# Kernel optimization log

Hardware: AMD Instinct MI355X
Metric: run time of the kernel (lower is better)

Reference implementation:

```python
import jax, jax.numpy as jnp
import numpy as np

R, B, S, H, E, P = 8, 16, 512, 1024, 32, 4  # roles, batch, seq(=max_seq_len=char_len), hidden, entities, spans/entity


def setup_inputs() -> dict:
    key = jax.random.key(0)
    ks = jax.random.split(key, 12)
    w = 0.02
    return {
        "role_labels": jax.random.randint(ks[0], (R, B), 0, S),
        "summar_role_embedding": jax.random.normal(ks[1], (R, B, S, H), jnp.float32),
        "token_embedding": jax.random.normal(ks[2], (B, S, H), jnp.float32),
        "entities_embedding": jax.random.normal(ks[3], (B, S, H), jnp.float32),
        "token_mask": jnp.ones((B, S), jnp.float32),
        "entity_mask": jnp.ones((B, S), jnp.float32),
        # padded ragged spans: sort (start,end) so start<=end; empty spans write nothing
        "entity_spans": jnp.sort(jax.random.randint(ks[4], (B, E, P, 2), 0, S), axis=-1),
        # -1 encodes Python None entries in the original ragged maps
        "char2token": jax.random.randint(ks[5], (B, S), -1, S),
        "entity2token": jax.random.randint(ks[6], (B, S), -1, E),
        "single_w": jax.random.normal(ks[7], (3 * H, 1), jnp.float32) * w,
        "single_b": jnp.zeros((1,), jnp.float32),
        "multi_w": jax.random.normal(ks[8], (3 * H, 1), jnp.float32) * w,
        "multi_b": jnp.zeros((1,), jnp.float32),
        "answer_w": jax.random.normal(ks[9], (2 * H, H), jnp.float32) * w,
        "answer_b": jnp.zeros((H,), jnp.float32),
    }


def reference(role_labels, summar_role_embedding, token_embedding, entities_embedding,
              token_mask, entity_mask, entity_spans, char2token, entity2token,
              single_w, single_b, multi_w, multi_b, answer_w, answer_b):
    Bd, Sd, Hd = token_embedding.shape
    Ed = entity_spans.shape[1]
    brow = jnp.arange(Bd)[:, None]
    cvalid = char2token >= 0
    cidx = jnp.where(cvalid, char2token, 0)
    evalid = entity2token >= 0
    eidx = jnp.where(evalid, entity2token, 0)
    pos = jnp.arange(Sd)[None, None, None, :]  # [1,1,1,S]
    # span coverage mask [B,E,P,S]; assumes non-overlapping gold spans (matches sequential writes)
    cover = ((pos >= entity_spans[..., 0:1]) & (pos < entity_spans[..., 1:2])).astype(token_embedding.dtype)
    mask_sum = token_mask.sum()

    def step(pre_answer, xs):
        sr_emb, labels = xs
        s_logit = jnp.concatenate([sr_emb, token_embedding, pre_answer], -1) @ single_w + single_b  # [B,S,1]
        m_logit = jnp.concatenate([sr_emb, entities_embedding, pre_answer], -1) @ multi_w + multi_b
        # nn.Softmax() with no dim on a 3D tensor uses legacy dim=0 (batch axis)
        s_pred = jax.nn.softmax(s_logit, axis=0)[..., 0]  # [B,S]
        m_pred = jax.nn.softmax(m_logit, axis=0)[..., 0]
        # scatter-add char scores onto token positions / entity ids
        pred_token_ids = jnp.zeros((Bd, Sd), s_pred.dtype).at[brow, cidx].add(jnp.where(cvalid, s_pred, 0.0))
        entity_scores = jnp.zeros((Bd, Ed), m_pred.dtype).at[brow, eidx].add(jnp.where(evalid, m_pred, 0.0))
        # broadcast entity score over its spans
        pred_entity_ids = jnp.einsum('beps,be->bs', cover, entity_scores)
        merged = jnp.maximum(pred_token_ids, pred_entity_ids)  # max-merge [B,S]
        # gather merged scores back to char positions
        arg_emb = jnp.where(cvalid, jnp.take_along_axis(merged, cidx, axis=1), 0.0)[..., None]  # [B,S,1]
        curr = token_embedding * arg_emb
        new_pre = jnp.concatenate([curr, pre_answer], -1) @ answer_w + answer_b
        # CrossEntropyLoss(merged [B,C=S], labels [B]) -> scalar mean, then * token_mask.sum()
        nll = -jnp.take_along_axis(jax.nn.log_softmax(merged, -1), labels[:, None], axis=1).mean()
        return new_pre, (merged, nll * mask_sum)

    pre0 = jnp.zeros_like(token_embedding)
    _, (pred_arg_ids, losses) = jax.lax.scan(step, pre0, (summar_role_embedding, role_labels))
    return losses.sum(), pred_arg_ids
```

## Files before the change

kernel.cpp:

```cpp
#include <hip/hip_runtime.h>
#include <stdint.h>

#define R_ 8
#define B_ 16
#define S_ 512
#define H_ 1024
#define E_ 32
#define P_ 4
#define M_ (B_*S_)
#define NWAVE_ 4096

__device__ __forceinline__ float dot4(float4 a, float4 b){
  return a.x*b.x + a.y*b.y + a.z*b.z + a.w*b.w;
}

__global__ __launch_bounds__(256) void vec_chain_kernel(
    int k, const float* __restrict__ aw, const float* __restrict__ ab,
    const float* __restrict__ sw, const float* __restrict__ mw,
    float* __restrict__ a_s, float* __restrict__ a_m,
    float* __restrict__ V, float* __restrict__ betas)
{
  int w = (int)((blockIdx.x * blockDim.x + threadIdx.x) >> 6);
  int lane = threadIdx.x & 63;
  const float* as_k = (k == 0) ? (sw + 2*H_) : (a_s + (size_t)k*H_);
  const float* am_k = (k == 0) ? (mw + 2*H_) : (a_m + (size_t)k*H_);
  if (w < H_){
    const float* w1 = aw + (size_t)w * H_;
    const float* w2 = aw + (size_t)(H_ + w) * H_;
    float vs = 0.f, vm = 0.f, ns = 0.f, nm = 0.f;
    #pragma unroll
    for (int i = 0; i < 4; i++){
      int c = i*256 + lane*4;
      float4 r1 = *(const float4*)(w1 + c);
      float4 r2 = *(const float4*)(w2 + c);
      float4 xs = *(const float4*)(as_k + c);
      float4 xm = *(const float4*)(am_k + c);
      vs += dot4(r1, xs); vm += dot4(r1, xm);
      ns += dot4(r2, xs); nm += dot4(r2, xm);
    }
    #pragma unroll
    for (int m = 32; m >= 1; m >>= 1){
      vs += __shfl_xor(vs, m, 64); vm += __shfl_xor(vm, m, 64);
      ns += __shfl_xor(ns, m, 64); nm += __shfl_xor(nm, m, 64);
    }
    if (lane == 0){
      V[(size_t)k*H_ + w]       = vs;
      V[(size_t)(7 + k)*H_ + w] = vm;
      a_s[(size_t)(k+1)*H_ + w] = ns;
      a_m[(size_t)(k+1)*H_ + w] = nm;
    }
  } else if (w == H_ || w == H_ + 1){
    const float* av = (w == H_) ? as_k : am_k;
    float d = 0.f;
    #pragma unroll
    for (int i = 0; i < 4; i++){
      int c = i*256 + lane*4;
      d += dot4(*(const float4*)(ab + c), *(const float4*)(av + c));
    }
    #pragma unroll
    for (int m = 32; m >= 1; m >>= 1) d += __shfl_xor(d, m, 64);
    if (lane == 0) betas[(w == H_ ? 0 : 8) + k] = d;
  }
}

__global__ __launch_bounds__(256, 4) void dots_all_kernel(
    const float* __restrict__ sr, const float* __restrict__ tok,
    const float* __restrict__ ent, const float* __restrict__ sw,
    const float* __restrict__ mw, const float* __restrict__ V,
    const float* __restrict__ tmask,
    float* __restrict__ sr_s, float* __restrict__ sr_m,
    float* __restrict__ tok_s, float* __restrict__ ent_m,
    float* __restrict__ G, float* __restrict__ PS,
    float* __restrict__ msum, float* __restrict__ out)
{
  const int gtid = blockIdx.x * 256 + threadIdx.x;
  const int gw   = gtid >> 6;
  const int lane = threadIdx.x & 63;
  const int co   = lane * 4;

  if (gtid < 32768) ((float4*)PS)[gtid] = make_float4(0.f,0.f,0.f,0.f);
  if (gw == 0){
    float s = 0.f;
    #pragma unroll
    for (int i = 0; i < 32; i++){
      float4 v = ((const float4*)tmask)[i*64 + lane];
      s += v.x + v.y + v.z + v.w;
    }
    #pragma unroll
    for (int m = 32; m >= 1; m >>= 1) s += __shfl_xor(s, m, 64);
    if (lane == 0){ msum[0] = s; out[0] = 0.f; }
  }

  {
    float4 ws[4], wm[4];
    #pragma unroll
    for (int i = 0; i < 4; i++){
      ws[i] = *(const float4*)(sw + i*256 + co);
      wm[i] = *(const float4*)(mw + i*256 + co);
    }
    float4 bufA[8], bufB[8];
    auto LDP = [&](float4* buf, int p){
      const float* r0 = sr + (size_t)p * (2*H_);
      #pragma unroll
      for (int i = 0; i < 4; i++){
        buf[i]   = *(const float4*)(r0 + i*256 + co);
        buf[4+i] = *(const float4*)(r0 + H_ + i*256 + co);
      }
    };
    auto CMP = [&](const float4* buf, int p){
      float a0=0.f,a1=0.f,b0=0.f,b1=0.f;
      #pragma unroll
      for (int i = 0; i < 4; i++){
        a0 += dot4(buf[i],   ws[i]);  a1 += dot4(buf[i],   wm[i]);
        b0 += dot4(buf[4+i], ws[i]);  b1 += dot4(buf[4+i], wm[i]);
      }
      #pragma unroll
      for (int m = 32; m >= 1; m >>= 1){
        a0 += __shfl_xor(a0,m,64); a1 += __shfl_xor(a1,m,64);
        b0 += __shfl_xor(b0,m,64); b1 += __shfl_xor(b1,m,64);
      }
      if (lane == 0){
        sr_s[2*p]   = a0; sr_m[2*p]   = a1;
        sr_s[2*p+1] = b0; sr_m[2*p+1] = b1;
      }
    };
    LDP(bufA, gw);
    #pragma unroll
    for (int it = 0; it < 8; it += 2){
      LDP(bufB, gw + (it+1)*NWAVE_);
      CMP(bufA, gw + it*NWAVE_);
      if (it + 2 < 8) LDP(bufA, gw + (it+2)*NWAVE_);
      CMP(bufB, gw + (it+1)*NWAVE_);
    }
  }

  {
    const int h  = gw & 1;
    const int r0 = gw >> 1;
    float4 vA[4], vB[4];
    auto LDV = [&](float4* v, int rr){
      const float* rp = tok + (size_t)rr * H_;
      #pragma unroll
      for (int i = 0; i < 4; i++) v[i] = *(const float4*)(rp + i*256 + co);
    };
    if (h == 0){
      auto CMP0 = [&](const float4* v, int rr){
        float acc[8] = {};
        #pragma unroll
        for (int i = 0; i < 4; i++){
          int c = i*256 + co;
          acc[0] += dot4(v[i], *(const float4*)(sw + H_ + c));
          #pragma unroll
          for (int q = 0; q < 7; q++)
            acc[q+1] += dot4(v[i], *(const float4*)(V + (size_t)q*H_ + c));
        }
        #pragma unroll
        for (int m = 32; m >= 1; m >>= 1)
          #pragma unroll
          for (int q = 0; q < 8; q++) acc[q] += __shfl_xor(acc[q],m,64);
        if (lane == 0){
          tok_s[rr] = acc[0];
          #pragma unroll
          for (int q = 0; q < 7; q++) G[(size_t)q*M_ + rr] = acc[q+1];
        }
      };
      LDV(vA, r0);
      LDV(vB, r0 + 2048); CMP0(vA, r0);
      LDV(vA, r0 + 4096); CMP0(vB, r0 + 2048);
      LDV(vB, r0 + 6144); CMP0(vA, r0 + 4096);
      CMP0(vB, r0 + 6144);
    } else {
      auto CMP1 = [&](const float4* v, int rr){
        float acc[7] = {};
        #pragma unroll
        for (int i = 0; i < 4; i++){
          int c = i*256 + co;
          #pragma unroll
          for (int q = 0; q < 7; q++)
            acc[q] += dot4(v[i], *(const float4*)(V + (size_t)(7+q)*H_ + c));
        }
        #pragma unroll
        for (int m = 32; m >= 1; m >>= 1)
          #pragma unroll
          for (int q = 0; q < 7; q++) acc[q] += __shfl_xor(acc[q],m,64);
        if (lane == 0){
          #pragma unroll
          for (int q = 0; q < 7; q++) G[(size_t)(7+q)*M_ + rr] = acc[q];
        }
      };
      LDV(vA, r0);
      LDV(vB, r0 + 2048); CMP1(vA, r0);
      LDV(vA, r0 + 4096); CMP1(vB, r0 + 2048);
      LDV(vB, r0 + 6144); CMP1(vA, r0 + 4096);
      CMP1(vB, r0 + 6144);
    }
  }

  {
    float4 wmh[4];
    #pragma unroll
    for (int i = 0; i < 4; i++) wmh[i] = *(const float4*)(mw + H_ + i*256 + co);
    float4 eA[4], eB[4];
    const float* rpA = ent + (size_t)gw * H_;
    const float* rpB = ent + (size_t)(gw + 4096) * H_;
    #pragma unroll
    for (int i = 0; i < 4; i++) eA[i] = *(const float4*)(rpA + i*256 + co);
    #pragma unroll
    for (int i = 0; i < 4; i++) eB[i] = *(const float4*)(rpB + i*256 + co);
    float a0 = 0.f, b0 = 0.f;
    #pragma unroll
    for (int i = 0; i < 4; i++){ a0 += dot4(eA[i], wmh[i]); b0 += dot4(eB[i], wmh[i]); }
    #pragma unroll
    for (int m = 32; m >= 1; m >>= 1){ a0 += __shfl_xor(a0,m,64); b0 += __shfl_xor(b0,m,64); }
    if (lane == 0){ ent_m[gw] = a0; ent_m[gw + 4096] = b0; }
  }
}

__global__ __launch_bounds__(512) void role_kernel(
    int r,
    const float* __restrict__ sr_s, const float* __restrict__ sr_m,
    const float* __restrict__ tok_s, const float* __restrict__ ent_m,
    const float* __restrict__ G, const float* __restrict__ betas,
    const float* __restrict__ sb, const float* __restrict__ mb,
    const int* __restrict__ c2t, const int* __restrict__ e2t,
    const int* __restrict__ spans, const int* __restrict__ labels,
    const float* __restrict__ msum, float* __restrict__ out,
    float* __restrict__ xlog, float* __restrict__ PS)
{
  __shared__ float pta[S_];
  __shared__ float merged[S_];
  __shared__ float es[E_];
  __shared__ float red[8];
  __shared__ int   spn[E_*P_*2];
  const int b = blockIdx.x;
  const int t = threadIdx.x;
  const int bs = b*S_ + t;
  const int wid = t >> 6, lane = t & 63;

  pta[t] = 0.f;
  if (t < E_) es[t] = 0.f;
  if (t < E_*P_*2) spn[t] = spans[b*(E_*P_*2) + t];
  const int c_own = c2t[bs];
  const int e_own = e2t[bs];

  float sl[B_], ml[B_];
  if (r == 0){
    const float sb0 = sb[0], mb0 = mb[0];
    #pragma unroll
    for (int bb = 0; bb < B_; bb++){
      int q = bb*S_ + t;
      sl[bb] = sr_s[q] + tok_s[q] + sb0;
      ml[bb] = sr_m[q] + ent_m[q] + mb0;
    }
  } else {
    const float* xc = xlog + (size_t)(r & 1) * (2*M_);
    #pragma unroll
    for (int bb = 0; bb < B_; bb++){
      sl[bb] = xc[bb*S_ + t];
      ml[bb] = xc[M_ + bb*S_ + t];
    }
  }
  float smax = -1e30f, mmax = -1e30f;
  #pragma unroll
  for (int bb = 0; bb < B_; bb++){ smax = fmaxf(smax, sl[bb]); mmax = fmaxf(mmax, ml[bb]); }
  float ssum = 0.f, msv = 0.f;
  #pragma unroll
  for (int bb = 0; bb < B_; bb++){ ssum += __expf(sl[bb]-smax); msv += __expf(ml[bb]-mmax); }
  float spv = __expf(sl[b]-smax) / ssum;
  float mpv = __expf(ml[b]-mmax) / msv;

  __syncthreads();
  if (c_own >= 0) atomicAdd(&pta[c_own], spv);
  if (e_own >= 0) atomicAdd(&es[e_own], mpv);
  __syncthreads();

  float pei = 0.f;
  #pragma unroll
  for (int e = 0; e < E_; e++){
    float sc = es[e];
    #pragma unroll
    for (int p = 0; p < P_; p++){
      int st = spn[e*8 + p*2], en = spn[e*8 + p*2 + 1];
      if (t >= st && t < en) pei += sc;
    }
  }
  float mg = fmaxf(pta[t], pei);
  merged[t] = mg;
  out[1 + (size_t)r*M_ + bs] = mg;
  __syncthreads();

  float ah_r = (c_own >= 0) ? merged[c_own] : 0.f;

  float mx = mg;
  #pragma unroll
  for (int k = 32; k >= 1; k >>= 1) mx = fmaxf(mx, __shfl_xor(mx, k, 64));
  if (lane == 0) red[wid] = mx;
  __syncthreads();
  float gmx = red[0];
  #pragma unroll
  for (int i = 1; i < 8; i++) gmx = fmaxf(gmx, red[i]);
  float se = __expf(mg - gmx);
  #pragma unroll
  for (int k = 32; k >= 1; k >>= 1) se += __shfl_xor(se, k, 64);
  __syncthreads();
  if (lane == 0) red[wid] = se;
  __syncthreads();
  if (t == 0){
    float tot = 0.f;
    #pragma unroll
    for (int i = 0; i < 8; i++) tot += red[i];
    float lse = gmx + __logf(tot);
    int lbl = labels[r*B_ + b];
    float nll = lse - merged[lbl];
    atomicAdd(out, nll * msum[0] * (1.0f/16.0f));
  }

  if (r < 7){
    float ps_next = 0.f, pm_next = 0.f;
    for (int q = r + 1; q <= 7; q++){
      float gs = G[(size_t)(q-1-r)*M_ + bs];
      float gm = G[(size_t)(7 + q-1-r)*M_ + bs];
      float ns = PS[((size_t)q*2 + 0)*M_ + bs] + ah_r * gs;
      float nm = PS[((size_t)q*2 + 1)*M_ + bs] + ah_r * gm;
      PS[((size_t)q*2 + 0)*M_ + bs] = ns;
      PS[((size_t)q*2 + 1)*M_ + bs] = nm;
      if (q == r + 1){ ps_next = ns; pm_next = nm; }
    }
    float bsum_s = 0.f, bsum_m = 0.f;
    for (int k = 0; k <= r; k++){ bsum_s += betas[k]; bsum_m += betas[8 + k]; }
    float xn = sr_s[(size_t)((r+1)*B_ + b)*S_ + t] + tok_s[bs] + ps_next + sb[0] + bsum_s;
    float yn = sr_m[(size_t)((r+1)*B_ + b)*S_ + t] + ent_m[bs] + pm_next + mb[0] + bsum_m;
    float* xn_buf = xlog + (size_t)((r+1) & 1) * (2*M_);
    xn_buf[bs] = xn;
    xn_buf[M_ + bs] = yn;
  }
}

extern "C" void kernel_launch(void* const* d_in, const int* in_sizes, int n_in,
                              void* d_out, int out_size, void* d_ws, size_t ws_size,
                              hipStream_t stream){
  (void)in_sizes; (void)n_in; (void)out_size; (void)ws_size;
  const int*   labels = (const int*)  d_in[0];
  const float* sr     = (const float*)d_in[1];
  const float* tok    = (const float*)d_in[2];
  const float* ent    = (const float*)d_in[3];
  const float* tmask  = (const float*)d_in[4];
  const int*   spans  = (const int*)  d_in[6];
  const int*   c2t    = (const int*)  d_in[7];
  const int*   e2t    = (const int*)  d_in[8];
  const float* sw     = (const float*)d_in[9];
  const float* sb     = (const float*)d_in[10];
  const float* mw     = (const float*)d_in[11];
  const float* mb     = (const float*)d_in[12];
  const float* aw     = (const float*)d_in[13];
  const float* ab     = (const float*)d_in[14];
  float* out = (float*)d_out;
  char*  ws  = (char*)d_ws;

  size_t o = 0;
  auto take = [&](size_t bytes){ size_t c = o; o += (bytes + 255) & ~(size_t)255; return c; };
  float* sr_s  = (float*)(ws + take((size_t)R_*B_*S_*4));
  float* sr_m  = (float*)(ws + take((size_t)R_*B_*S_*4));
  float* tok_s = (float*)(ws + take((size_t)B_*S_*4));
  float* ent_m = (float*)(ws + take((size_t)B_*S_*4));
  float* a_s   = (float*)(ws + take((size_t)8*H_*4));
  float* a_m   = (float*)(ws + take((size_t)8*H_*4));
  float* V     = (float*)(ws + take((size_t)14*H_*4));
  float* betas = (float*)(ws + take(64));
  float* G     = (float*)(ws + take((size_t)14*M_*4));
  float* PS    = (float*)(ws + take((size_t)8*2*M_*4));
  float* xlog  = (float*)(ws + take((size_t)2*2*M_*4));
  float* msum  = (float*)(ws + take(256));

  for (int k = 0; k < 7; k++)
    vec_chain_kernel<<<257, 256, 0, stream>>>(k, aw, ab, sw, mw, a_s, a_m, V, betas);
  dots_all_kernel<<<1024, 256, 0, stream>>>(sr, tok, ent, sw, mw, V, tmask,
                                            sr_s, sr_m, tok_s, ent_m, G, PS, msum, out);
  for (int r = 0; r < R_; r++){
    role_kernel<<<16, 512, 0, stream>>>(r, sr_s, sr_m, tok_s, ent_m, G, betas,
                                        sb, mb, c2t, e2t, spans, labels, msum, out,
                                        xlog, PS);
  }
}
```

Measured before the change: 187.0 us.

## Fuse vector chain into streaming kernel with grid barriers; persistent role loop

Folds the seven sequential vec_chain launches into a mega kernel: 64 blocks run the matrix-vector chain with software grid barriers, then compute the token dot products against V. The remaining blocks stream the role and entity embeddings at the same time. The eight role launches become one persistent 16-block kernel that loops over roles with an inter-block barrier. This removes about fifteen launch gaps and overlaps the dependent chain with bandwidth-bound work. The cost is spin-wait barriers that assume all blocks are co-resident, and fewer waves left for the token dot products.

New measurement: 487.5 us. 2.61x slower.

```diff
diff --git a/kernel.cpp b/kernel.cpp
--- a/kernel.cpp
+++ b/kernel.cpp
@@ -8,95 +8,140 @@
 #define E_ 32
 #define P_ 4
 #define M_ (B_*S_)
-#define NWAVE_ 4096
+#define CHAINB_ 64
+#define TOTB_ 1024
+#define SRW_ ((TOTB_-CHAINB_)*4)
 
 __device__ __forceinline__ float dot4(float4 a, float4 b){
   return a.x*b.x + a.y*b.y + a.z*b.z + a.w*b.w;
 }
 
-__global__ __launch_bounds__(256) void vec_chain_kernel(
-    int k, const float* __restrict__ aw, const float* __restrict__ ab,
-    const float* __restrict__ sw, const float* __restrict__ mw,
-    float* __restrict__ a_s, float* __restrict__ a_m,
-    float* __restrict__ V, float* __restrict__ betas)
-{
-  int w = (int)((blockIdx.x * blockDim.x + threadIdx.x) >> 6);
-  int lane = threadIdx.x & 63;
-  const float* as_k = (k == 0) ? (sw + 2*H_) : (a_s + (size_t)k*H_);
-  const float* am_k = (k == 0) ? (mw + 2*H_) : (a_m + (size_t)k*H_);
-  if (w < H_){
-    const float* w1 = aw + (size_t)w * H_;
-    const float* w2 = aw + (size_t)(H_ + w) * H_;
-    float vs = 0.f, vm = 0.f, ns = 0.f, nm = 0.f;
-    #pragma unroll
-    for (int i = 0; i < 4; i++){
-      int c = i*256 + lane*4;
-      float4 r1 = *(const float4*)(w1 + c);
-      float4 r2 = *(const float4*)(w2 + c);
-      float4 xs = *(const float4*)(as_k + c);
-      float4 xm = *(const float4*)(am_k + c);
-      vs += dot4(r1, xs); vm += dot4(r1, xm);
-      ns += dot4(r2, xs); nm += dot4(r2, xm);
-    }
-    #pragma unroll
-    for (int m = 32; m >= 1; m >>= 1){
-      vs += __shfl_xor(vs, m, 64); vm += __shfl_xor(vm, m, 64);
-      ns += __shfl_xor(ns, m, 64); nm += __shfl_xor(nm, m, 64);
-    }
-    if (lane == 0){
-      V[(size_t)k*H_ + w]       = vs;
-      V[(size_t)(7 + k)*H_ + w] = vm;
-      a_s[(size_t)(k+1)*H_ + w] = ns;
-      a_m[(size_t)(k+1)*H_ + w] = nm;
-    }
-  } else if (w == H_ || w == H_ + 1){
-    const float* av = (w == H_) ? as_k : am_k;
-    float d = 0.f;
-    #pragma unroll
-    for (int i = 0; i < 4; i++){
-      int c = i*256 + lane*4;
-      d += dot4(*(const float4*)(ab + c), *(const float4*)(av + c));
-    }
-    #pragma unroll
-    for (int m = 32; m >= 1; m >>= 1) d += __shfl_xor(d, m, 64);
-    if (lane == 0) betas[(w == H_ ? 0 : 8) + k] = d;
+__device__ __forceinline__ void group_barrier(int* cnt, int nblk){
+  __syncthreads();
+  if (threadIdx.x == 0){
+    __threadfence();
+    __hip_atomic_fetch_add(cnt, 1, __ATOMIC_RELEASE, __HIP_MEMORY_SCOPE_AGENT);
+    while (__hip_atomic_load(cnt, __ATOMIC_ACQUIRE, __HIP_MEMORY_SCOPE_AGENT) < nblk)
+      __builtin_amdgcn_s_sleep(8);
+    __threadfence();
   }
-}
-
-__global__ __launch_bounds__(256, 4) void dots_all_kernel(
+  __syncthreads();
+}
+
+__global__ __launch_bounds__(256, 4) void mega_kernel(
     const float* __restrict__ sr, const float* __restrict__ tok,
     const float* __restrict__ ent, const float* __restrict__ sw,
-    const float* __restrict__ mw, const float* __restrict__ V,
-    const float* __restrict__ tmask,
+    const float* __restrict__ mw, const float* __restrict__ aw,
+    const float* __restrict__ ab, const float* __restrict__ tmask,
     float* __restrict__ sr_s, float* __restrict__ sr_m,
     float* __restrict__ tok_s, float* __restrict__ ent_m,
+    float* __restrict__ a_s, float* __restrict__ a_m,
+    float* __restrict__ V, float* __restrict__ betas,
     float* __restrict__ G, float* __restrict__ PS,
-    float* __restrict__ msum, float* __restrict__ out)
+    float* __restrict__ msum, float* __restrict__ out, int* bar)
 {
-  const int gtid = blockIdx.x * 256 + threadIdx.x;
-  const int gw   = gtid >> 6;
+  const int blk  = blockIdx.x;
   const int lane = threadIdx.x & 63;
+  const int lw   = threadIdx.x >> 6;
   const int co   = lane * 4;
 
-  if (gtid < 32768) ((float4*)PS)[gtid] = make_float4(0.f,0.f,0.f,0.f);
-  if (gw == 0){
-    float s = 0.f;
-    #pragma unroll
-    for (int i = 0; i < 32; i++){
-      float4 v = ((const float4*)tmask)[i*64 + lane];
-      s += v.x + v.y + v.z + v.w;
-    }
-    #pragma unroll
-    for (int m = 32; m >= 1; m >>= 1) s += __shfl_xor(s, m, 64);
-    if (lane == 0){ msum[0] = s; out[0] = 0.f; }
-  }
-
-  {
-    float4 ws[4], wm[4];
+  if (blk < CHAINB_){
+    const int cw = blk*4 + lw;
+    for (int k = 0; k < 7; ++k){
+      const float* as_k = (k==0) ? (sw + 2*H_) : (a_s + (size_t)k*H_);
+      const float* am_k = (k==0) ? (mw + 2*H_) : (a_m + (size_t)k*H_);
+      float4 xs[4], xm[4];
+      #pragma unroll
+      for (int i = 0; i < 4; i++){
+        xs[i] = *(const float4*)(as_k + i*256 + co);
+        xm[i] = *(const float4*)(am_k + i*256 + co);
+      }
+      #pragma unroll
+      for (int rr = 0; rr < 4; ++rr){
+        int w = cw*4 + rr;
+        const float* w1 = aw + (size_t)w * H_;
+        const float* w2 = aw + (size_t)(H_ + w) * H_;
+        float vs=0.f, vm=0.f, ns=0.f, nm=0.f;
+        #pragma unroll
+        for (int i = 0; i < 4; i++){
+          float4 r1 = *(const float4*)(w1 + i*256 + co);
+          float4 r2 = *(const float4*)(w2 + i*256 + co);
+          vs += dot4(r1, xs[i]); vm += dot4(r1, xm[i]);
+          ns += dot4(r2, xs[i]); nm += dot4(r2, xm[i]);
+        }
+        #pragma unroll
+        for (int m = 32; m >= 1; m >>= 1){
+          vs += __shfl_xor(vs,m,64); vm += __shfl_xor(vm,m,64);
+          ns += __shfl_xor(ns,m,64); nm += __shfl_xor(nm,m,64);
+        }
+        if (lane == 0){
+          V[(size_t)k*H_ + w]       = vs;
+          V[(size_t)(7+k)*H_ + w]   = vm;
+          a_s[(size_t)(k+1)*H_ + w] = ns;
+          a_m[(size_t)(k+1)*H_ + w] = nm;
+        }
+      }
+      if (cw == 0){
+        float d0=0.f, d1=0.f;
+        #pragma unroll
+        for (int i = 0; i < 4; i++){
+          float4 r = *(const float4*)(ab + i*256 + co);
+          d0 += dot4(r, xs[i]); d1 += dot4(r, xm[i]);
+        }
+        #pragma unroll
+        for (int m = 32; m >= 1; m >>= 1){ d0+=__shfl_xor(d0,m,64); d1+=__shfl_xor(d1,m,64); }
+        if (lane == 0){ betas[k] = d0; betas[8+k] = d1; }
+      }
+      group_barrier(&bar[k], CHAINB_);
+    }
+    for (int it = 0; it < 32; ++it){
+      int rr = cw + it*256;
+      const float* rp = tok + (size_t)rr * H_;
+      float4 v[4];
+      #pragma unroll
+      for (int i = 0; i < 4; i++) v[i] = *(const float4*)(rp + i*256 + co);
+      float acc[15];
+      #pragma unroll
+      for (int q = 0; q < 15; q++) acc[q] = 0.f;
+      #pragma unroll
+      for (int i = 0; i < 4; i++){
+        int c = i*256 + co;
+        acc[0] += dot4(v[i], *(const float4*)(sw + H_ + c));
+        #pragma unroll
+        for (int q = 0; q < 14; q++)
+          acc[q+1] += dot4(v[i], *(const float4*)(V + (size_t)q*H_ + c));
+      }
+      #pragma unroll
+      for (int m = 32; m >= 1; m >>= 1)
+        #pragma unroll
+        for (int q = 0; q < 15; q++) acc[q] += __shfl_xor(acc[q],m,64);
+      if (lane == 0){
+        tok_s[rr] = acc[0];
+        #pragma unroll
+        for (int q = 0; q < 14; q++) G[(size_t)q*M_ + rr] = acc[q+1];
+      }
+    }
+  } else {
+    const int sb   = blk - CHAINB_;
+    const int swv  = sb*4 + lw;
+    const int gtid2 = sb*256 + threadIdx.x;
+    if (gtid2 < 32768) ((float4*)PS)[gtid2] = make_float4(0.f,0.f,0.f,0.f);
+    if (swv == 0){
+      float s = 0.f;
+      #pragma unroll
+      for (int i = 0; i < 32; i++){
+        float4 vv = ((const float4*)tmask)[i*64 + lane];
+        s += vv.x + vv.y + vv.z + vv.w;
+      }
+      #pragma unroll
+      for (int m = 32; m >= 1; m >>= 1) s += __shfl_xor(s,m,64);
+      if (lane == 0){ msum[0] = s; out[0] = 0.f; }
+    }
+    float4 ws4[4], wm4[4];
     #pragma unroll
     for (int i = 0; i < 4; i++){
-      ws[i] = *(const float4*)(sw + i*256 + co);
-      wm[i] = *(const float4*)(mw + i*256 + co);
+      ws4[i] = *(const float4*)(sw + i*256 + co);
+      wm4[i] = *(const float4*)(mw + i*256 + co);
     }
     float4 bufA[8], bufB[8];
     auto LDP = [&](float4* buf, int p){
@@ -111,113 +156,51 @@
       float a0=0.f,a1=0.f,b0=0.f,b1=0.f;
       #pragma unroll
       for (int i = 0; i < 4; i++){
-        a0 += dot4(buf[i],   ws[i]);  a1 += dot4(buf[i],   wm[i]);
-        b0 += dot4(buf[4+i], ws[i]);  b1 += dot4(buf[4+i], wm[i]);
+        a0 += dot4(buf[i],   ws4[i]);  a1 += dot4(buf[i],   wm4[i]);
+        b0 += dot4(buf[4+i], ws4[i]);  b1 += dot4(buf[4+i], wm4[i]);
       }
       #pragma unroll
       for (int m = 32; m >= 1; m >>= 1){
-        a0 += __shfl_xor(a0,m,64); a1 += __shfl_xor(a1,m,64);
-        b0 += __shfl_xor(b0,m,64); b1 += __shfl_xor(b1,m,64);
+        a0+=__shfl_xor(a0,m,64); a1+=__shfl_xor(a1,m,64);
+        b0+=__shfl_xor(b0,m,64); b1+=__shfl_xor(b1,m,64);
       }
       if (lane == 0){
         sr_s[2*p]   = a0; sr_m[2*p]   = a1;
         sr_s[2*p+1] = b0; sr_m[2*p+1] = b1;
       }
     };
-    LDP(bufA, gw);
-    #pragma unroll
-    for (int it = 0; it < 8; it += 2){
-      LDP(bufB, gw + (it+1)*NWAVE_);
-      CMP(bufA, gw + it*NWAVE_);
-      if (it + 2 < 8) LDP(bufA, gw + (it+2)*NWAVE_);
-      CMP(bufB, gw + (it+1)*NWAVE_);
+    int p = swv;
+    LDP(bufA, p);
+    while (true){
+      int pn = p + SRW_;
+      bool more = (pn < 32768);
+      if (more) LDP(bufB, pn);
+      CMP(bufA, p);
+      if (!more) break;
+      p = pn; pn = p + SRW_;
+      more = (pn < 32768);
+      if (more) LDP(bufA, pn);
+      CMP(bufB, p);
+      if (!more) break;
+      p = pn;
+    }
+    float4 wmh[4];
+    #pragma unroll
+    for (int i = 0; i < 4; i++) wmh[i] = *(const float4*)(mw + H_ + i*256 + co);
+    for (int rr = swv; rr < B_*S_; rr += SRW_){
+      const float* rp = ent + (size_t)rr * H_;
+      float a0 = 0.f;
+      #pragma unroll
+      for (int i = 0; i < 4; i++)
+        a0 += dot4(*(const float4*)(rp + i*256 + co), wmh[i]);
+      #pragma unroll
+      for (int m = 32; m >= 1; m >>= 1) a0 += __shfl_xor(a0,m,64);
+      if (lane == 0) ent_m[rr] = a0;
     }
   }
-
-  {
-    const int h  = gw & 1;
-    const int r0 = gw >> 1;
-    float4 vA[4], vB[4];
-    auto LDV = [&](float4* v, int rr){
-      const float* rp = tok + (size_t)rr * H_;
-      #pragma unroll
-      for (int i = 0; i < 4; i++) v[i] = *(const float4*)(rp + i*256 + co);
-    };
-    if (h == 0){
-      auto CMP0 = [&](const float4* v, int rr){
-        float acc[8] = {};
-        #pragma unroll
-        for (int i = 0; i < 4; i++){
-          int c = i*256 + co;
-          acc[0] += dot4(v[i], *(const float4*)(sw + H_ + c));
-          #pragma unroll
-          for (int q = 0; q < 7; q++)
-            acc[q+1] += dot4(v[i], *(const float4*)(V + (size_t)q*H_ + c));
-        }
-        #pragma unroll
-        for (int m = 32; m >= 1; m >>= 1)
-          #pragma unroll
-          for (int q = 0; q < 8; q++) acc[q] += __shfl_xor(acc[q],m,64);
-        if (lane == 0){
-          tok_s[rr] = acc[0];
-          #pragma unroll
-          for (int q = 0; q < 7; q++) G[(size_t)q*M_ + rr] = acc[q+1];
-        }
-      };
-      LDV(vA, r0);
-      LDV(vB, r0 + 2048); CMP0(vA, r0);
-      LDV(vA, r0 + 4096); CMP0(vB, r0 + 2048);
-      LDV(vB, r0 + 6144); CMP0(vA, r0 + 4096);
-      CMP0(vB, r0 + 6144);
-    } else {
-      auto CMP1 = [&](const float4* v, int rr){
-        float acc[7] = {};
-        #pragma unroll
-        for (int i = 0; i < 4; i++){
-          int c = i*256 + co;
-          #pragma unroll
-          for (int q = 0; q < 7; q++)
-            acc[q] += dot4(v[i], *(const float4*)(V + (size_t)(7+q)*H_ + c));
-        }
-        #pragma unroll
-        for (int m = 32; m >= 1; m >>= 1)
-          #pragma unroll
-          for (int q = 0; q < 7; q++) acc[q] += __shfl_xor(acc[q],m,64);
-        if (lane == 0){
-          #pragma unroll
-          for (int q = 0; q < 7; q++) G[(size_t)(7+q)*M_ + rr] = acc[q];
-        }
-      };
-      LDV(vA, r0);
-      LDV(vB, r0 + 2048); CMP1(vA, r0);
-      LDV(vA, r0 + 4096); CMP1(vB, r0 + 2048);
-      LDV(vB, r0 + 6144); CMP1(vA, r0 + 4096);
-      CMP1(vB, r0 + 6144);
-    }
-  }
-
-  {
-    float4 wmh[4];
-    #pragma unroll
-    for (int i = 0; i < 4; i++) wmh[i] = *(const float4*)(mw + H_ + i*256 + co);
-    float4 eA[4], eB[4];
-    const float* rpA = ent + (size_t)gw * H_;
-    const float* rpB = ent + (size_t)(gw + 4096) * H_;
-    #pragma unroll
-    for (int i = 0; i < 4; i++) eA[i] = *(const float4*)(rpA + i*256 + co);
-    #pragma unroll
-    for (int i = 0; i < 4; i++) eB[i] = *(const float4*)(rpB + i*256 + co);
-    float a0 = 0.f, b0 = 0.f;
-    #pragma unroll
-    for (int i = 0; i < 4; i++){ a0 += dot4(eA[i], wmh[i]); b0 += dot4(eB[i], wmh[i]); }
-    #pragma unroll
-    for (int m = 32; m >= 1; m >>= 1){ a0 += __shfl_xor(a0,m,64); b0 += __shfl_xor(b0,m,64); }
-    if (lane == 0){ ent_m[gw] = a0; ent_m[gw + 4096] = b0; }
-  }
-}
-
-__global__ __launch_bounds__(512) void role_kernel(
-    int r,
+}
+
+__global__ __launch_bounds__(512) void roles_kernel(
     const float* __restrict__ sr_s, const float* __restrict__ sr_m,
     const float* __restrict__ tok_s, const float* __restrict__ ent_m,
     const float* __restrict__ G, const float* __restrict__ betas,
@@ -225,7 +208,7 @@
     const int* __restrict__ c2t, const int* __restrict__ e2t,
     const int* __restrict__ spans, const int* __restrict__ labels,
     const float* __restrict__ msum, float* __restrict__ out,
-    float* __restrict__ xlog, float* __restrict__ PS)
+    float* __restrict__ xlog, float* __restrict__ PS, int* bar)
 {
   __shared__ float pta[S_];
   __shared__ float merged[S_];
@@ -237,102 +220,108 @@
   const int bs = b*S_ + t;
   const int wid = t >> 6, lane = t & 63;
 
-  pta[t] = 0.f;
-  if (t < E_) es[t] = 0.f;
   if (t < E_*P_*2) spn[t] = spans[b*(E_*P_*2) + t];
   const int c_own = c2t[bs];
   const int e_own = e2t[bs];
-
-  float sl[B_], ml[B_];
-  if (r == 0){
-    const float sb0 = sb[0], mb0 = mb[0];
-    #pragma unroll
-    for (int bb = 0; bb < B_; bb++){
-      int q = bb*S_ + t;
-      sl[bb] = sr_s[q] + tok_s[q] + sb0;
-      ml[bb] = sr_m[q] + ent_m[q] + mb0;
-    }
-  } else {
-    const float* xc = xlog + (size_t)(r & 1) * (2*M_);
-    #pragma unroll
-    for (int bb = 0; bb < B_; bb++){
-      sl[bb] = xc[bb*S_ + t];
-      ml[bb] = xc[M_ + bb*S_ + t];
-    }
-  }
-  float smax = -1e30f, mmax = -1e30f;
-  #pragma unroll
-  for (int bb = 0; bb < B_; bb++){ smax = fmaxf(smax, sl[bb]); mmax = fmaxf(mmax, ml[bb]); }
-  float ssum = 0.f, msv = 0.f;
-  #pragma unroll
-  for (int bb = 0; bb < B_; bb++){ ssum += __expf(sl[bb]-smax); msv += __expf(ml[bb]-mmax); }
-  float spv = __expf(sl[b]-smax) / ssum;
-  float mpv = __expf(ml[b]-mmax) / msv;
-
-  __syncthreads();
-  if (c_own >= 0) atomicAdd(&pta[c_own], spv);
-  if (e_own >= 0) atomicAdd(&es[e_own], mpv);
-  __syncthreads();
-
-  float pei = 0.f;
-  #pragma unroll
-  for (int e = 0; e < E_; e++){
-    float sc = es[e];
-    #pragma unroll
-    for (int p = 0; p < P_; p++){
-      int st = spn[e*8 + p*2], en = spn[e*8 + p*2 + 1];
-      if (t >= st && t < en) pei += sc;
-    }
-  }
-  float mg = fmaxf(pta[t], pei);
-  merged[t] = mg;
-  out[1 + (size_t)r*M_ + bs] = mg;
-  __syncthreads();
-
-  float ah_r = (c_own >= 0) ? merged[c_own] : 0.f;
-
-  float mx = mg;
-  #pragma unroll
-  for (int k = 32; k >= 1; k >>= 1) mx = fmaxf(mx, __shfl_xor(mx, k, 64));
-  if (lane == 0) red[wid] = mx;
-  __syncthreads();
-  float gmx = red[0];
-  #pragma unroll
-  for (int i = 1; i < 8; i++) gmx = fmaxf(gmx, red[i]);
-  float se = __expf(mg - gmx);
-  #pragma unroll
-  for (int k = 32; k >= 1; k >>= 1) se += __shfl_xor(se, k, 64);
-  __syncthreads();
-  if (lane == 0) red[wid] = se;
-  __syncthreads();
-  if (t == 0){
-    float tot = 0.f;
-    #pragma unroll
-    for (int i = 0; i < 8; i++) tot += red[i];
-    float lse = gmx + __logf(tot);
-    int lbl = labels[r*B_ + b];
-    float nll = lse - merged[lbl];
-    atomicAdd(out, nll * msum[0] * (1.0f/16.0f));
-  }
-
-  if (r < 7){
-    float ps_next = 0.f, pm_next = 0.f;
-    for (int q = r + 1; q <= 7; q++){
-      float gs = G[(size_t)(q-1-r)*M_ + bs];
-      float gm = G[(size_t)(7 + q-1-r)*M_ + bs];
-      float ns = PS[((size_t)q*2 + 0)*M_ + bs] + ah_r * gs;
-      float nm = PS[((size_t)q*2 + 1)*M_ + bs] + ah_r * gm;
-      PS[((size_t)q*2 + 0)*M_ + bs] = ns;
-      PS[((size_t)q*2 + 1)*M_ + bs] = nm;
-      if (q == r + 1){ ps_next = ns; pm_next = nm; }
-    }
-    float bsum_s = 0.f, bsum_m = 0.f;
-    for (int k = 0; k <= r; k++){ bsum_s += betas[k]; bsum_m += betas[8 + k]; }
-    float xn = sr_s[(size_t)((r+1)*B_ + b)*S_ + t] + tok_s[bs] + ps_next + sb[0] + bsum_s;
-    float yn = sr_m[(size_t)((r+1)*B_ + b)*S_ + t] + ent_m[bs] + pm_next + mb[0] + bsum_m;
-    float* xn_buf = xlog + (size_t)((r+1) & 1) * (2*M_);
-    xn_buf[bs] = xn;
-    xn_buf[M_ + bs] = yn;
+  const float sb0 = sb[0], mb0 = mb[0];
+  const float msumv = msum[0];
+  const float tok_sv = tok_s[bs], ent_mv = ent_m[bs];
+  float bsum_s = 0.f, bsum_m = 0.f;
+
+  for (int r = 0; r < R_; ++r){
+    pta[t] = 0.f;
+    if (t < E_) es[t] = 0.f;
+
+    float sl[B_], ml[B_];
+    if (r == 0){
+      #pragma unroll
+      for (int bb = 0; bb < B_; bb++){
+        int q = bb*S_ + t;
+        sl[bb] = sr_s[q] + tok_s[q] + sb0;
+        ml[bb] = sr_m[q] + ent_m[q] + mb0;
+      }
+    } else {
+      const float* xc = xlog + (size_t)(r & 1) * (2*M_);
+      #pragma unroll
+      for (int bb = 0; bb < B_; bb++){
+        sl[bb] = xc[bb*S_ + t];
+        ml[bb] = xc[M_ + bb*S_ + t];
+      }
+    }
+    float smax = -1e30f, mmax = -1e30f;
+    #pragma unroll
+    for (int bb = 0; bb < B_; bb++){ smax = fmaxf(smax, sl[bb]); mmax = fmaxf(mmax, ml[bb]); }
+    float ssum = 0.f, msv = 0.f;
+    #pragma unroll
+    for (int bb = 0; bb < B_; bb++){ ssum += __expf(sl[bb]-smax); msv += __expf(ml[bb]-mmax); }
+    float spv = __expf(sl[b]-smax) / ssum;
+    float mpv = __expf(ml[b]-mmax) / msv;
+
+    __syncthreads();
+    if (c_own >= 0) atomicAdd(&pta[c_own], spv);
+    if (e_own >= 0) atomicAdd(&es[e_own], mpv);
+    __syncthreads();
+
+    float pei = 0.f;
+    #pragma unroll
+    for (int e = 0; e < E_; e++){
+      float sc = es[e];
+      #pragma unroll
+      for (int p = 0; p < P_; p++){
+        int st = spn[e*8 + p*2], en = spn[e*8 + p*2 + 1];
+        if (t >= st && t < en) pei += sc;
+      }
+    }
+    float mg = fmaxf(pta[t], pei);
+    merged[t] = mg;
+    out[1 + (size_t)r*M_ + bs] = mg;
+    __syncthreads();
+
+    float ah_r = (c_own >= 0) ? merged[c_own] : 0.f;
+
+    float mx = mg;
+    #pragma unroll
+    for (int k = 32; k >= 1; k >>= 1) mx = fmaxf(mx, __shfl_xor(mx, k, 64));
+    if (lane == 0) red[wid] = mx;
+    __syncthreads();
+    float gmx = red[0];
+    #pragma unroll
+    for (int i = 1; i < 8; i++) gmx = fmaxf(gmx, red[i]);
+    float se = __expf(mg - gmx);
+    #pragma unroll
+    for (int k = 32; k >= 1; k >>= 1) se += __shfl_xor(se, k, 64);
+    __syncthreads();
+    if (lane == 0) red[wid] = se;
+    __syncthreads();
+    if (t == 0){
+      float tot = 0.f;
+      #pragma unroll
+      for (int i = 0; i < 8; i++) tot += red[i];
+      float lse = gmx + __logf(tot);
+      int lbl = labels[r*B_ + b];
+      float nll = lse - merged[lbl];
+      atomicAdd(out, nll * msumv * (1.0f/16.0f));
+    }
+
+    if (r < 7){
+      bsum_s += betas[r]; bsum_m += betas[8 + r];
+      float ps_next = 0.f, pm_next = 0.f;
+      for (int q = r + 1; q <= 7; q++){
+        float gs = G[(size_t)(q-1-r)*M_ + bs];
+        float gm = G[(size_t)(7 + q-1-r)*M_ + bs];
+        float ns = PS[((size_t)q*2 + 0)*M_ + bs] + ah_r * gs;
+        float nm = PS[((size_t)q*2 + 1)*M_ + bs] + ah_r * gm;
+        PS[((size_t)q*2 + 0)*M_ + bs] = ns;
+        PS[((size_t)q*2 + 1)*M_ + bs] = nm;
+        if (q == r + 1){ ps_next = ns; pm_next = nm; }
+      }
+      float xn = sr_s[(size_t)((r+1)*B_ + b)*S_ + t] + tok_sv + ps_next + sb0 + bsum_s;
+      float yn = sr_m[(size_t)((r+1)*B_ + b)*S_ + t] + ent_mv + pm_next + mb0 + bsum_m;
+      float* xn_buf = xlog + (size_t)((r+1) & 1) * (2*M_);
+      xn_buf[bs] = xn;
+      xn_buf[M_ + bs] = yn;
+      group_barrier(&bar[8 + r], 16);
+    }
   }
 }
 
@@ -371,14 +360,13 @@
   float* PS    = (float*)(ws + take((size_t)8*2*M_*4));
   float* xlog  = (float*)(ws + take((size_t)2*2*M_*4));
   float* msum  = (float*)(ws + take(256));
-
-  for (int k = 0; k < 7; k++)
-    vec_chain_kernel<<<257, 256, 0, stream>>>(k, aw, ab, sw, mw, a_s, a_m, V, betas);
-  dots_all_kernel<<<1024, 256, 0, stream>>>(sr, tok, ent, sw, mw, V, tmask,
-                                            sr_s, sr_m, tok_s, ent_m, G, PS, msum, out);
-  for (int r = 0; r < R_; r++){
-    role_kernel<<<16, 512, 0, stream>>>(r, sr_s, sr_m, tok_s, ent_m, G, betas,
-                                        sb, mb, c2t, e2t, spans, labels, msum, out,
-                                        xlog, PS);
-  }
-}
+  int*   bar   = (int*)  (ws + take(64));
+
+  hipMemsetAsync(bar, 0, 64, stream);
+  mega_kernel<<<TOTB_, 256, 0, stream>>>(sr, tok, ent, sw, mw, aw, ab, tmask,
+                                         sr_s, sr_m, tok_s, ent_m, a_s, a_m,
+                                         V, betas, G, PS, msum, out, bar);
+  roles_kernel<<<16, 512, 0, stream>>>(sr_s, sr_m, tok_s, ent_m, G, betas,
+                                       sb, mb, c2t, e2t, spans, labels, msum, out,
+                                       xlog, PS, bar);
+}
```

## Fuse per-role launches into one persistent kernel with grid barrier; double dots grid

Applied to the files above, without the earlier changes.

Replaces the eight sequential role_kernel launches with a single 16-block persistent kernel that loops over roles and synchronises blocks through an atomic counter barrier in workspace. The aim is to remove per-launch overhead and gaps along the serial role chain. It also reworks dots_all_kernel to launch twice as many blocks, with each wave handling fewer rows and no explicit software double-buffering, and raises the occupancy hint. The spin barrier assumes all 16 blocks are co-resident and adds a memset launch to reset the counters.

New measurement: 197.6 us. +5.7%, slower.

```diff
diff --git a/kernel.cpp b/kernel.cpp
--- a/kernel.cpp
+++ b/kernel.cpp
@@ -8,10 +8,21 @@
 #define E_ 32
 #define P_ 4
 #define M_ (B_*S_)
-#define NWAVE_ 4096
 
 __device__ __forceinline__ float dot4(float4 a, float4 b){
   return a.x*b.x + a.y*b.y + a.z*b.z + a.w*b.w;
+}
+
+__device__ __forceinline__ void group_barrier(int* cnt, int nblk){
+  __syncthreads();
+  if (threadIdx.x == 0){
+    __threadfence();
+    __hip_atomic_fetch_add(cnt, 1, __ATOMIC_RELEASE, __HIP_MEMORY_SCOPE_AGENT);
+    while (__hip_atomic_load(cnt, __ATOMIC_ACQUIRE, __HIP_MEMORY_SCOPE_AGENT) < nblk)
+      __builtin_amdgcn_s_sleep(8);
+    __threadfence();
+  }
+  __syncthreads();
 }
 
 __global__ __launch_bounds__(256) void vec_chain_kernel(
@@ -63,7 +74,7 @@
   }
 }
 
-__global__ __launch_bounds__(256, 4) void dots_all_kernel(
+__global__ __launch_bounds__(256, 6) void dots_all_kernel(
     const float* __restrict__ sr, const float* __restrict__ tok,
     const float* __restrict__ ent, const float* __restrict__ sw,
     const float* __restrict__ mw, const float* __restrict__ V,
@@ -92,67 +103,50 @@
   }
 
   {
-    float4 ws[4], wm[4];
+    float4 ws4[4], wm4[4];
     #pragma unroll
     for (int i = 0; i < 4; i++){
-      ws[i] = *(const float4*)(sw + i*256 + co);
-      wm[i] = *(const float4*)(mw + i*256 + co);
-    }
-    float4 bufA[8], bufB[8];
-    auto LDP = [&](float4* buf, int p){
-      const float* r0 = sr + (size_t)p * (2*H_);
+      ws4[i] = *(const float4*)(sw + i*256 + co);
+      wm4[i] = *(const float4*)(mw + i*256 + co);
+    }
+    #pragma unroll
+    for (int it = 0; it < 8; ++it){
+      int w = gw + it*8192;
+      const float* rp = sr + (size_t)w * H_;
+      float a0 = 0.f, a1 = 0.f;
       #pragma unroll
       for (int i = 0; i < 4; i++){
-        buf[i]   = *(const float4*)(r0 + i*256 + co);
-        buf[4+i] = *(const float4*)(r0 + H_ + i*256 + co);
-      }
-    };
-    auto CMP = [&](const float4* buf, int p){
-      float a0=0.f,a1=0.f,b0=0.f,b1=0.f;
-      #pragma unroll
-      for (int i = 0; i < 4; i++){
-        a0 += dot4(buf[i],   ws[i]);  a1 += dot4(buf[i],   wm[i]);
-        b0 += dot4(buf[4+i], ws[i]);  b1 += dot4(buf[4+i], wm[i]);
+        float4 v = *(const float4*)(rp + i*256 + co);
+        a0 += dot4(v, ws4[i]);
+        a1 += dot4(v, wm4[i]);
       }
       #pragma unroll
       for (int m = 32; m >= 1; m >>= 1){
         a0 += __shfl_xor(a0,m,64); a1 += __shfl_xor(a1,m,64);
-        b0 += __shfl_xor(b0,m,64); b1 += __shfl_xor(b1,m,64);
-      }
-      if (lane == 0){
-        sr_s[2*p]   = a0; sr_m[2*p]   = a1;
-        sr_s[2*p+1] = b0; sr_m[2*p+1] = b1;
-      }
-    };
-    LDP(bufA, gw);
-    #pragma unroll
-    for (int it = 0; it < 8; it += 2){
-      LDP(bufB, gw + (it+1)*NWAVE_);
-      CMP(bufA, gw + it*NWAVE_);
-      if (it + 2 < 8) LDP(bufA, gw + (it+2)*NWAVE_);
-      CMP(bufB, gw + (it+1)*NWAVE_);
+      }
+      if (lane == 0){ sr_s[w] = a0; sr_m[w] = a1; }
     }
   }
 
   {
     const int h  = gw & 1;
     const int r0 = gw >> 1;
-    float4 vA[4], vB[4];
-    auto LDV = [&](float4* v, int rr){
-      const float* rp = tok + (size_t)rr * H_;
-      #pragma unroll
-      for (int i = 0; i < 4; i++) v[i] = *(const float4*)(rp + i*256 + co);
-    };
     if (h == 0){
-      auto CMP0 = [&](const float4* v, int rr){
-        float acc[8] = {};
+      #pragma unroll
+      for (int it = 0; it < 2; ++it){
+        int rr = r0 + it*4096;
+        const float* rp = tok + (size_t)rr * H_;
+        float acc[8];
+        #pragma unroll
+        for (int q = 0; q < 8; q++) acc[q] = 0.f;
         #pragma unroll
         for (int i = 0; i < 4; i++){
           int c = i*256 + co;
-          acc[0] += dot4(v[i], *(const float4*)(sw + H_ + c));
+          float4 v = *(const float4*)(rp + c);
+          acc[0] += dot4(v, *(const float4*)(sw + H_ + c));
           #pragma unroll
           for (int q = 0; q < 7; q++)
-            acc[q+1] += dot4(v[i], *(const float4*)(V + (size_t)q*H_ + c));
+            acc[q+1] += dot4(v, *(const float4*)(V + (size_t)q*H_ + c));
         }
         #pragma unroll
         for (int m = 32; m >= 1; m >>= 1)
@@ -163,21 +157,22 @@
           #pragma unroll
           for (int q = 0; q < 7; q++) G[(size_t)q*M_ + rr] = acc[q+1];
         }
-      };
-      LDV(vA, r0);
-      LDV(vB, r0 + 2048); CMP0(vA, r0);
-      LDV(vA, r0 + 4096); CMP0(vB, r0 + 2048);
-      LDV(vB, r0 + 6144); CMP0(vA, r0 + 4096);
-      CMP0(vB, r0 + 6144);
+      }
     } else {
-      auto CMP1 = [&](const float4* v, int rr){
-        float acc[7] = {};
+      #pragma unroll
+      for (int it = 0; it < 2; ++it){
+        int rr = r0 + it*4096;
+        const float* rp = tok + (size_t)rr * H_;
+        float acc[7];
+        #pragma unroll
+        for (int q = 0; q < 7; q++) acc[q] = 0.f;
         #pragma unroll
         for (int i = 0; i < 4; i++){
           int c = i*256 + co;
+          float4 v = *(const float4*)(rp + c);
           #pragma unroll
           for (int q = 0; q < 7; q++)
-            acc[q] += dot4(v[i], *(const float4*)(V + (size_t)(7+q)*H_ + c));
+            acc[q] += dot4(v, *(const float4*)(V + (size_t)(7+q)*H_ + c));
         }
         #pragma unroll
         for (int m = 32; m >= 1; m >>= 1)
@@ -187,37 +182,25 @@
           #pragma unroll
           for (int q = 0; q < 7; q++) G[(size_t)(7+q)*M_ + rr] = acc[q];
         }
-      };
-      LDV(vA, r0);
-      LDV(vB, r0 + 2048); CMP1(vA, r0);
-      LDV(vA, r0 + 4096); CMP1(vB, r0 + 2048);
-      LDV(vB, r0 + 6144); CMP1(vA, r0 + 4096);
-      CMP1(vB, r0 + 6144);
+      }
     }
   }
 
   {
-    float4 wmh[4];
-    #pragma unroll
-    for (int i = 0; i < 4; i++) wmh[i] = *(const float4*)(mw + H_ + i*256 + co);
-    float4 eA[4], eB[4];
-    const float* rpA = ent + (size_t)gw * H_;
-    const float* rpB = ent + (size_t)(gw + 4096) * H_;
-    #pragma unroll
-    for (int i = 0; i < 4; i++) eA[i] = *(const float4*)(rpA + i*256 + co);
-    #pragma unroll
-    for (int i = 0; i < 4; i++) eB[i] = *(const float4*)(rpB + i*256 + co);
-    float a0 = 0.f, b0 = 0.f;
-    #pragma unroll
-    for (int i = 0; i < 4; i++){ a0 += dot4(eA[i], wmh[i]); b0 += dot4(eB[i], wmh[i]); }
-    #pragma unroll
-    for (int m = 32; m >= 1; m >>= 1){ a0 += __shfl_xor(a0,m,64); b0 += __shfl_xor(b0,m,64); }
-    if (lane == 0){ ent_m[gw] = a0; ent_m[gw + 4096] = b0; }
-  }
-}
-
-__global__ __launch_bounds__(512) void role_kernel(
-    int r,
+    const float* rp = ent + (size_t)gw * H_;
+    float a0 = 0.f;
+    #pragma unroll
+    for (int i = 0; i < 4; i++){
+      float4 v = *(const float4*)(rp + i*256 + co);
+      a0 += dot4(v, *(const float4*)(mw + H_ + i*256 + co));
+    }
+    #pragma unroll
+    for (int m = 32; m >= 1; m >>= 1) a0 += __shfl_xor(a0,m,64);
+    if (lane == 0) ent_m[gw] = a0;
+  }
+}
+
+__global__ __launch_bounds__(512) void roles_kernel(
     const float* __restrict__ sr_s, const float* __restrict__ sr_m,
     const float* __restrict__ tok_s, const float* __restrict__ ent_m,
     const float* __restrict__ G, const float* __restrict__ betas,
@@ -225,7 +208,7 @@
     const int* __restrict__ c2t, const int* __restrict__ e2t,
     const int* __restrict__ spans, const int* __restrict__ labels,
     const float* __restrict__ msum, float* __restrict__ out,
-    float* __restrict__ xlog, float* __restrict__ PS)
+    float* __restrict__ xlog, float* __restrict__ PS, int* bar)
 {
   __shared__ float pta[S_];
   __shared__ float merged[S_];
@@ -237,102 +220,108 @@
   const int bs = b*S_ + t;
   const int wid = t >> 6, lane = t & 63;
 
-  pta[t] = 0.f;
-  if (t < E_) es[t] = 0.f;
   if (t < E_*P_*2) spn[t] = spans[b*(E_*P_*2) + t];
   const int c_own = c2t[bs];
   const int e_own = e2t[bs];
-
-  float sl[B_], ml[B_];
-  if (r == 0){
-    const float sb0 = sb[0], mb0 = mb[0];
-    #pragma unroll
-    for (int bb = 0; bb < B_; bb++){
-      int q = bb*S_ + t;
-      sl[bb] = sr_s[q] + tok_s[q] + sb0;
-      ml[bb] = sr_m[q] + ent_m[q] + mb0;
-    }
-  } else {
-    const float* xc = xlog + (size_t)(r & 1) * (2*M_);
-    #pragma unroll
-    for (int bb = 0; bb < B_; bb++){
-      sl[bb] = xc[bb*S_ + t];
-      ml[bb] = xc[M_ + bb*S_ + t];
-    }
-  }
-  float smax = -1e30f, mmax = -1e30f;
-  #pragma unroll
-  for (int bb = 0; bb < B_; bb++){ smax = fmaxf(smax, sl[bb]); mmax = fmaxf(mmax, ml[bb]); }
-  float ssum = 0.f, msv = 0.f;
-  #pragma unroll
-  for (int bb = 0; bb < B_; bb++){ ssum += __expf(sl[bb]-smax); msv += __expf(ml[bb]-mmax); }
-  float spv = __expf(sl[b]-smax) / ssum;
-  float mpv = __expf(ml[b]-mmax) / msv;
-
-  __syncthreads();
-  if (c_own >= 0) atomicAdd(&pta[c_own], spv);
-  if (e_own >= 0) atomicAdd(&es[e_own], mpv);
-  __syncthreads();
-
-  float pei = 0.f;
-  #pragma unroll
-  for (int e = 0; e < E_; e++){
-    float sc = es[e];
-    #pragma unroll
-    for (int p = 0; p < P_; p++){
-      int st = spn[e*8 + p*2], en = spn[e*8 + p*2 + 1];
-      if (t >= st && t < en) pei += sc;
-    }
-  }
-  float mg = fmaxf(pta[t], pei);
-  merged[t] = mg;
-  out[1 + (size_t)r*M_ + bs] = mg;
-  __syncthreads();
-
-  float ah_r = (c_own >= 0) ? merged[c_own] : 0.f;
-
-  float mx = mg;
-  #pragma unroll
-  for (int k = 32; k >= 1; k >>= 1) mx = fmaxf(mx, __shfl_xor(mx, k, 64));
-  if (lane == 0) red[wid] = mx;
-  __syncthreads();
-  float gmx = red[0];
-  #pragma unroll
-  for (int i = 1; i < 8; i++) gmx = fmaxf(gmx, red[i]);
-  float se = __expf(mg - gmx);
-  #pragma unroll
-  for (int k = 32; k >= 1; k >>= 1) se += __shfl_xor(se, k, 64);
-  __syncthreads();
-  if (lane == 0) red[wid] = se;
-  __syncthreads();
-  if (t == 0){
-    float tot = 0.f;
-    #pragma unroll
-    for (int i = 0; i < 8; i++) tot += red[i];
-    float lse = gmx + __logf(tot);
-    int lbl = labels[r*B_ + b];
-    float nll = lse - merged[lbl];
-    atomicAdd(out, nll * msum[0] * (1.0f/16.0f));
-  }
-
-  if (r < 7){
-    float ps_next = 0.f, pm_next = 0.f;
-    for (int q = r + 1; q <= 7; q++){
-      float gs = G[(size_t)(q-1-r)*M_ + bs];
-      float gm = G[(size_t)(7 + q-1-r)*M_ + bs];
-      float ns = PS[((size_t)q*2 + 0)*M_ + bs] + ah_r * gs;
-      float nm = PS[((size_t)q*2 + 1)*M_ + bs] + ah_r * gm;
-      PS[((size_t)q*2 + 0)*M_ + bs] = ns;
-      PS[((size_t)q*2 + 1)*M_ + bs] = nm;
-      if (q == r + 1){ ps_next = ns; pm_next = nm; }
-    }
-    float bsum_s = 0.f, bsum_m = 0.f;
-    for (int k = 0; k <= r; k++){ bsum_s += betas[k]; bsum_m += betas[8 + k]; }
-    float xn = sr_s[(size_t)((r+1)*B_ + b)*S_ + t] + tok_s[bs] + ps_next + sb[0] + bsum_s;
-    float yn = sr_m[(size_t)((r+1)*B_ + b)*S_ + t] + ent_m[bs] + pm_next + mb[0] + bsum_m;
-    float* xn_buf = xlog + (size_t)((r+1) & 1) * (2*M_);
-    xn_buf[bs] = xn;
-    xn_buf[M_ + bs] = yn;
+  const float sb0 = sb[0], mb0 = mb[0];
+  const float msumv = msum[0];
+  const float tok_sv = tok_s[bs], ent_mv = ent_m[bs];
+  float bsum_s = 0.f, bsum_m = 0.f;
+
+  for (int r = 0; r < R_; ++r){
+    pta[t] = 0.f;
+    if (t < E_) es[t] = 0.f;
+
+    float sl[B_], ml[B_];
+    if (r == 0){
+      #pragma unroll
+      for (int bb = 0; bb < B_; bb++){
+        int q = bb*S_ + t;
+        sl[bb] = sr_s[q] + tok_s[q] + sb0;
+        ml[bb] = sr_m[q] + ent_m[q] + mb0;
+      }
+    } else {
+      const float* xc = xlog + (size_t)(r & 1) * (2*M_);
+      #pragma unroll
+      for (int bb = 0; bb < B_; bb++){
+        sl[bb] = xc[bb*S_ + t];
+        ml[bb] = xc[M_ + bb*S_ + t];
+      }
+    }
+    float smax = -1e30f, mmax = -1e30f;
+    #pragma unroll
+    for (int bb = 0; bb < B_; bb++){ smax = fmaxf(smax, sl[bb]); mmax = fmaxf(mmax, ml[bb]); }
+    float ssum = 0.f, msv = 0.f;
+    #pragma unroll
+    for (int bb = 0; bb < B_; bb++){ ssum += __expf(sl[bb]-smax); msv += __expf(ml[bb]-mmax); }
+    float spv = __expf(sl[b]-smax) / ssum;
+    float mpv = __expf(ml[b]-mmax) / msv;
+
+    __syncthreads();
+    if (c_own >= 0) atomicAdd(&pta[c_own], spv);
+    if (e_own >= 0) atomicAdd(&es[e_own], mpv);
+    __syncthreads();
+
+    float pei = 0.f;
+    #pragma unroll
+    for (int e = 0; e < E_; e++){
+      float sc = es[e];
+      #pragma unroll
+      for (int p = 0; p < P_; p++){
+        int st = spn[e*8 + p*2], en = spn[e*8 + p*2 + 1];
+        if (t >= st && t < en) pei += sc;
+      }
+    }
+    float mg = fmaxf(pta[t], pei);
+    merged[t] = mg;
+    out[1 + (size_t)r*M_ + bs] = mg;
+    __syncthreads();
+
+    float ah_r = (c_own >= 0) ? merged[c_own] : 0.f;
+
+    float mx = mg;
+    #pragma unroll
+    for (int k = 32; k >= 1; k >>= 1) mx = fmaxf(mx, __shfl_xor(mx, k, 64));
+    if (lane == 0) red[wid] = mx;
+    __syncthreads();
+    float gmx = red[0];
+    #pragma unroll
+    for (int i = 1; i < 8; i++) gmx = fmaxf(gmx, red[i]);
+    float se = __expf(mg - gmx);
+    #pragma unroll
+    for (int k = 32; k >= 1; k >>= 1) se += __shfl_xor(se, k, 64);
+    __syncthreads();
+    if (lane == 0) red[wid] = se;
+    __syncthreads();
+    if (t == 0){
+      float tot = 0.f;
+      #pragma unroll
+      for (int i = 0; i < 8; i++) tot += red[i];
+      float lse = gmx + __logf(tot);
+      int lbl = labels[r*B_ + b];
+      float nll = lse - merged[lbl];
+      atomicAdd(out, nll * msumv * (1.0f/16.0f));
+    }
+
+    if (r < 7){
+      bsum_s += betas[r]; bsum_m += betas[8 + r];
+      float ps_next = 0.f, pm_next = 0.f;
+      for (int q = r + 1; q <= 7; q++){
+        float gs = G[(size_t)(q-1-r)*M_ + bs];
+        float gm = G[(size_t)(7 + q-1-r)*M_ + bs];
+        float ns = PS[((size_t)q*2 + 0)*M_ + bs] + ah_r * gs;
+        float nm = PS[((size_t)q*2 + 1)*M_ + bs] + ah_r * gm;
+        PS[((size_t)q*2 + 0)*M_ + bs] = ns;
+        PS[((size_t)q*2 + 1)*M_ + bs] = nm;
+        if (q == r + 1){ ps_next = ns; pm_next = nm; }
+      }
+      float xn = sr_s[(size_t)((r+1)*B_ + b)*S_ + t] + tok_sv + ps_next + sb0 + bsum_s;
+      float yn = sr_m[(size_t)((r+1)*B_ + b)*S_ + t] + ent_mv + pm_next + mb0 + bsum_m;
+      float* xn_buf = xlog + (size_t)((r+1) & 1) * (2*M_);
+      xn_buf[bs] = xn;
+      xn_buf[M_ + bs] = yn;
+      group_barrier(&bar[r], 16);
+    }
   }
 }
 
@@ -371,14 +360,14 @@
   float* PS    = (float*)(ws + take((size_t)8*2*M_*4));
   float* xlog  = (float*)(ws + take((size_t)2*2*M_*4));
   float* msum  = (float*)(ws + take(256));
-
+  int*   bar   = (int*)  (ws + take(64));
+
+  hipMemsetAsync(bar, 0, 64, stream);
   for (int k = 0; k < 7; k++)
     vec_chain_kernel<<<257, 256, 0, stream>>>(k, aw, ab, sw, mw, a_s, a_m, V, betas);
-  dots_all_kernel<<<1024, 256, 0, stream>>>(sr, tok, ent, sw, mw, V, tmask,
+  dots_all_kernel<<<2048, 256, 0, stream>>>(sr, tok, ent, sw, mw, V, tmask,
                                             sr_s, sr_m, tok_s, ent_m, G, PS, msum, out);
-  for (int r = 0; r < R_; r++){
-    role_kernel<<<16, 512, 0, stream>>>(r, sr_s, sr_m, tok_s, ent_m, G, betas,
-                                        sb, mb, c2t, e2t, spans, labels, msum, out,
-                                        xlog, PS);
-  }
-}
+  roles_kernel<<<16, 512, 0, stream>>>(sr_s, sr_m, tok_s, ent_m, G, betas,
+                                       sb, mb, c2t, e2t, spans, labels, msum, out,
+                                       xlog, PS, bar);
+}
```
